# Performance work log

Measured on AMD Instinct MI355X. Metric: run time of the kernel, lower is better.

## Reference

```python
import jax, jax.numpy as jnp
from jax import lax
import numpy as np

SCALE = 3.0
TOPK = 16  # eigvec[:, -16:] in the original module
BN_EPS = 1e-5
DN = ('NCHW', 'OIHW', 'NCHW')


def setup_inputs() -> dict:
    key = jax.random.key(0)
    ks = jax.random.split(key, 8)
    B, C, H, W = 16, 256, 64, 64
    x = jax.random.normal(ks[0], (B, C, H, W), dtype=jnp.float32)
    conv1_w = jax.random.normal(ks[1], (C, C, 1, 1), dtype=jnp.float32) * (1.0 / np.sqrt(C))
    conv1_b = jax.random.normal(ks[2], (C,), dtype=jnp.float32) * 0.01
    conv2_w = jax.random.normal(ks[3], (C, C, 3, 3), dtype=jnp.float32) * (1.0 / np.sqrt(9 * C))
    bn_gamma = jnp.ones((C,), dtype=jnp.float32)
    bn_beta = jnp.zeros((C,), dtype=jnp.float32)
    bn_mean = jax.random.normal(ks[4], (C,), dtype=jnp.float32) * 0.1
    bn_var = jax.random.uniform(ks[5], (C,), dtype=jnp.float32, minval=0.5, maxval=1.5)
    return {"x": x, "conv1_w": conv1_w, "conv1_b": conv1_b, "conv2_w": conv2_w,
            "bn_gamma": bn_gamma, "bn_beta": bn_beta, "bn_mean": bn_mean, "bn_var": bn_var}


def reference(x, conv1_w, conv1_b, conv2_w, bn_gamma, bn_beta, bn_mean, bn_var):
    B, C, H, W = x.shape
    # conv1: 1x1 conv with bias
    gx = lax.conv_general_dilated(x, conv1_w, (1, 1), 'SAME', dimension_numbers=DN)
    gx = gx + conv1_b[None, :, None, None]
    # center over spatial positions: [B, C, N]
    g = gx.reshape(B, C, H * W)
    g = g - jnp.mean(g, axis=-1, keepdims=True)
    # per-batch covariance, divided by batch size (faithful to original gx.shape[0])
    cmat = jnp.einsum('bcn,bdn->bcd', g, g) / B  # [B, C, C]
    # batched symmetric eigendecomposition (ascending eigenvalues, like torch.symeig)
    _, vecs = jnp.linalg.eigh(cmat)              # vecs: [B, C, C]
    w = jnp.swapaxes(vecs[..., -TOPK:], -1, -2)  # top-16 eigvecs, [B, 16, C]
    # project onto eigvec subspace, softmax over the 16 components (dim=1)
    z = jax.nn.softmax(jnp.einsum('bkc,bcn->bkn', w, g) * SCALE, axis=1)  # [B, 16, N]
    y = jnp.einsum('bkc,bkn->bcn', w, z).reshape(B, C, H, W)
    # conv2: 3x3 conv (no bias) + BatchNorm (eval mode with running stats)
    att = lax.conv_general_dilated(y, conv2_w, (1, 1), 'SAME', dimension_numbers=DN)
    inv = bn_gamma * lax.rsqrt(bn_var + BN_EPS)
    att = att * inv[None, :, None, None] + (bn_beta - bn_mean * inv)[None, :, None, None]
    return x + att
```

## Files before the change

kernel.cpp:

```cpp
#include <hip/hip_runtime.h>
#include <hip/hip_bf16.h>
#include <math.h>


typedef __hip_bfloat16 bf16;

#define NB 16
#define NC 256
#define NSP 4096
#define LAPACK_EPS32 5.9604644775390625e-08

#define PHB_I0 80
#define PHB_M  176

__device__ __forceinline__ float b2f(bf16 v){ return __bfloat162float(v); }
__device__ __forceinline__ double safelog(double x){
  double a = fabs(x);
  if (!(a > 0.0) || !isfinite(a)) a = 1e-300;
  return log(a);
}

__device__ __forceinline__ float blk_reduce_sum(float s, float* red, int tid){
  red[tid] = s; __syncthreads();
  if (tid < 128) red[tid] += red[tid+128];
  __syncthreads();
  if (tid < 64){
    float x = red[tid] + red[tid+64];
    #pragma unroll
    for (int o = 32; o > 0; o >>= 1) x += __shfl_down(x, o);
    if (tid == 0) red[0] = x;
  }
  __syncthreads();
  return red[0];
}

__global__ __launch_bounds__(256) void k_detect(const unsigned short* __restrict__ xr,
                                                int* __restrict__ flags){
  __shared__ int red[256];
  int tid = threadIdx.x;
  int cnt = 0;
  for (int i = tid; i < 4096; i += 256){
    unsigned int u = xr[i];
    unsigned int e = (u >> 7) & 0xFF;
    if (e >= 134) ++cnt;
  }
  red[tid] = cnt; __syncthreads();
  for (int o=128;o>0;o>>=1){ if(tid<o) red[tid]+=red[tid+o]; __syncthreads(); }
  if (tid==0) flags[0] = (red[0] > 50) ? 1 : 0;
}

__global__ __launch_bounds__(256) void k_conv1(const void* __restrict__ xv_,
                                               const void* __restrict__ w1v,
                                               const int* __restrict__ flags,
                                               float* __restrict__ g){
  __shared__ float ws[16][256];
  int nt = blockIdx.x, ct = blockIdx.y, b = blockIdx.z;
  int tid = threadIdx.x;
  int c0 = ct*16;
  int isf = flags[0];
  if (isf){
    const float* w1 = (const float*)w1v;
    for (int i = tid; i < 16*256; i += 256)
      ws[i>>8][i&255] = w1[(size_t)(c0 + (i>>8))*256 + (i&255)];
  } else {
    const bf16* w1 = (const bf16*)w1v;
    for (int i = tid; i < 16*256; i += 256)
      ws[i>>8][i&255] = b2f(w1[(size_t)(c0 + (i>>8))*256 + (i&255)]);
  }
  __syncthreads();
  int n = nt*256 + tid;
  float acc[16];
  #pragma unroll
  for (int i=0;i<16;++i) acc[i]=0.f;
  if (isf){
    const float* xp = (const float*)xv_ + (size_t)b*NC*NSP + n;
    for (int d=0; d<256; ++d){
      float xv = xp[(size_t)d*NSP];
      #pragma unroll
      for (int i=0;i<16;++i) acc[i] = fmaf(ws[i][d], xv, acc[i]);
    }
  } else {
    const bf16* xp = (const bf16*)xv_ + (size_t)b*NC*NSP + n;
    for (int d=0; d<256; ++d){
      float xv = b2f(xp[(size_t)d*NSP]);
      #pragma unroll
      for (int i=0;i<16;++i) acc[i] = fmaf(ws[i][d], xv, acc[i]);
    }
  }
  float* gp = g + ((size_t)b*NC + c0)*NSP + n;
  #pragma unroll
  for (int i=0;i<16;++i) gp[(size_t)i*NSP] = acc[i];
}

__global__ __launch_bounds__(256) void k_center(float* __restrict__ g){
  int bc = blockIdx.x;
  float* p = g + (size_t)bc*NSP;
  int tid = threadIdx.x;
  __shared__ float red[256];
  float s = 0.f;
  for (int i=tid;i<NSP;i+=256) s += p[i];
  red[tid]=s; __syncthreads();
  for (int o=128;o>0;o>>=1){ if(tid<o) red[tid]+=red[tid+o]; __syncthreads(); }
  float mean = red[0] * (1.0f/4096.0f);
  for (int i=tid;i<NSP;i+=256) p[i] -= mean;
}

__global__ __launch_bounds__(256) void k_cmat(const float* __restrict__ g,
                                              float* __restrict__ A){
  __shared__ float t1[32][65];
  __shared__ float t2[32][65];
  int bx = blockIdx.x, by = blockIdx.y, b = blockIdx.z;
  int tid = threadIdx.x;
  int tx = tid & 31, ty = tid >> 5;
  const float* gb = g + (size_t)b*NC*NSP;
  float acc[4] = {0.f,0.f,0.f,0.f};
  for (int ch=0; ch<64; ++ch){
    int n0 = ch*64;
    for (int idx=tid; idx<2048; idx+=256){
      int r = idx>>6, cc = idx&63;
      t1[r][cc] = gb[(size_t)(by*32 + r)*NSP + n0 + cc];
      t2[r][cc] = gb[(size_t)(bx*32 + r)*NSP + n0 + cc];
    }
    __syncthreads();
    for (int kk=0; kk<64; ++kk){
      float v2 = t2[tx][kk];
      #pragma unroll
      for (int jj=0;jj<4;++jj) acc[jj] = fmaf(t1[ty+8*jj][kk], v2, acc[jj]);
    }
    __syncthreads();
  }
  #pragma unroll
  for (int jj=0;jj<4;++jj){
    int row = by*32 + ty + 8*jj, col = bx*32 + tx;
    A[((size_t)b*NC + row)*NC + col] = acc[jj]*(1.0f/16.0f);
  }
}

__global__ __launch_bounds__(256,1) void k_sytd2(float* __restrict__ Ag,
                                                 float* __restrict__ e_g,
                                                 float* __restrict__ tau_g,
                                                 float* __restrict__ d_g){
  int b = blockIdx.x, tid = threadIdx.x;
  float* A = Ag + (size_t)b*65536;
  __shared__ float Asub[PHB_M*PHB_M];
  __shared__ float v[256], wv[256], red[256];

  for (int i=0;i<PHB_I0;++i){
    float alpha = A[(size_t)i*256+(i+1)];
    float s=0.f;
    for (int r=i+2+tid; r<256; r+=256){ float a=A[(size_t)i*256+r]; s+=a*a; }
    float xnorm2 = blk_reduce_sum(s, red, tid);
    float tau=0.f, scale=0.f, beta=alpha;
    if (xnorm2 > 0.f){
      float r_ = sqrtf(alpha*alpha + xnorm2);
      beta = (alpha >= 0.f) ? -r_ : r_;
      tau = (beta - alpha)/beta;
      scale = 1.0f/(alpha - beta);
    }
    if (tid==0){ e_g[b*256+i] = beta; tau_g[b*256+i] = tau; }
    if (tau != 0.f){
      for (int r=i+1+tid; r<256; r+=256){
        float val = (r==i+1)?1.0f : A[(size_t)i*256+r]*scale;
        A[(size_t)i*256+r] = val;  v[r] = val;
      }
      __syncthreads();
      for (int r=i+1+tid; r<256; r+=256){
        const float* Ar = A + r;
        float acc=0.f;
        int base = i+1;
        int nfull = (256-base) >> 5;
        float b0[32], b1[32];
        if (nfull>0){
          #pragma unroll
          for (int u=0;u<32;++u) b0[u] = Ar[(size_t)(base+u)*256];
        }
        int t=0;
        for (; t+2<=nfull; t+=2){
          int cB = base+(t+1)*32;
          #pragma unroll
          for (int u=0;u<32;++u) b1[u] = Ar[(size_t)(cB+u)*256];
          int cA = base+t*32;
          #pragma unroll
          for (int u=0;u<32;++u) acc = fmaf(b0[u], v[cA+u], acc);
          if (t+2 < nfull){
            int cC = base+(t+2)*32;
            #pragma unroll
            for (int u=0;u<32;++u) b0[u] = Ar[(size_t)(cC+u)*256];
          }
          #pragma unroll
          for (int u=0;u<32;++u) acc = fmaf(b1[u], v[cB+u], acc);
        }
        if (t<nfull){
          int cA = base+t*32;
          #pragma unroll
          for (int u=0;u<32;++u) acc = fmaf(b0[u], v[cA+u], acc);
          ++t;
        }
        for (int c2=base+nfull*32; c2<256; ++c2) acc = fmaf(Ar[(size_t)c2*256], v[c2], acc);
        wv[r] = tau*acc;
      }
      __syncthreads();
      float sd=0.f;
      for (int r=i+1+tid;r<256;r+=256) sd += v[r]*wv[r];
      float dotv = blk_reduce_sum(sd, red, tid);
      float a2 = -0.5f*tau*dotv;
      for (int r=i+1+tid;r<256;r+=256) wv[r] += a2*v[r];
      __syncthreads();
      int r = i+1+tid;
      if (r < 256){
        float vr=v[r], wr=wv[r];
        float* Arw = A + r;
        int base=i+1;
        int nfull=(256-base)>>5;
        float b0[32], b1[32];
        if (nfull>0){
          #pragma unroll
          for (int u=0;u<32;++u) b0[u] = Arw[(size_t)(base+u)*256];
        }
        int t=0;
        for (; t+2<=nfull; t+=2){
          int cB = base+(t+1)*32;
          #pragma unroll
          for (int u=0;u<32;++u) b1[u] = Arw[(size_t)(cB+u)*256];
          int cA = base+t*32;
          #pragma unroll
          for (int u=0;u<32;++u) b0[u] -= vr*wv[cA+u] + wr*v[cA+u];
          #pragma unroll
          for (int u=0;u<32;++u) Arw[(size_t)(cA+u)*256] = b0[u];
          if (t+2 < nfull){
            int cC = base+(t+2)*32;
            #pragma unroll
            for (int u=0;u<32;++u) b0[u] = Arw[(size_t)(cC+u)*256];
          }
          #pragma unroll
          for (int u=0;u<32;++u) b1[u] -= vr*wv[cB+u] + wr*v[cB+u];
          #pragma unroll
          for (int u=0;u<32;++u) Arw[(size_t)(cB+u)*256] = b1[u];
        }
        if (t<nfull){
          int cA = base+t*32;
          #pragma unroll
          for (int u=0;u<32;++u) b0[u] -= vr*wv[cA+u] + wr*v[cA+u];
          #pragma unroll
          for (int u=0;u<32;++u) Arw[(size_t)(cA+u)*256] = b0[u];
          ++t;
        }
        for (int c2=base+nfull*32; c2<256; ++c2)
          Arw[(size_t)c2*256] -= vr*wv[c2] + wr*v[c2];
      }
      __syncthreads();
    }
    __syncthreads();
  }

  for (int idx=tid; idx<PHB_M*PHB_M; idx+=256){
    int cc = idx / PHB_M, rr = idx - cc*PHB_M;
    Asub[idx] = A[(size_t)(PHB_I0+cc)*256 + (PHB_I0+rr)];
  }
  __syncthreads();

  for (int i=PHB_I0;i<255;++i){
    int cb = (i - PHB_I0)*PHB_M;
    float alpha = Asub[cb + (i+1-PHB_I0)];
    float s=0.f;
    for (int r=i+2+tid; r<256; r+=256){ float a=Asub[cb + (r-PHB_I0)]; s+=a*a; }
    float xnorm2 = blk_reduce_sum(s, red, tid);
    float tau=0.f, scale=0.f, beta=alpha;
    if (xnorm2 > 0.f){
      float r_ = sqrtf(alpha*alpha + xnorm2);
      beta = (alpha >= 0.f) ? -r_ : r_;
      tau = (beta - alpha)/beta;
      scale = 1.0f/(alpha - beta);
    }
    if (tid==0){ e_g[b*256+i] = beta; tau_g[b*256+i] = tau; }
    if (tau != 0.f){
      for (int r=i+1+tid; r<256; r+=256){
        float val = (r==i+1)?1.0f : Asub[cb+(r-PHB_I0)]*scale;
        Asub[cb+(r-PHB_I0)] = val;
        A[(size_t)i*256+r] = val;
        v[r] = val;
      }
      __syncthreads();
      for (int r=i+1+tid; r<256; r+=256){
        int ro = r - PHB_I0;
        float acc=0.f;
        int base=i+1;
        int nfull=(256-base)>>4;
        for (int t=0;t<nfull;++t){
          int cA = base + t*16;
          float av[16];
          #pragma unroll
          for (int u=0;u<16;++u) av[u] = Asub[(cA+u-PHB_I0)*PHB_M + ro];
          #pragma unroll
          for (int u=0;u<16;++u) acc = fmaf(av[u], v[cA+u], acc);
        }
        for (int c2=base+nfull*16;c2<256;++c2)
          acc = fmaf(Asub[(c2-PHB_I0)*PHB_M+ro], v[c2], acc);
        wv[r] = tau*acc;
      }
      __syncthreads();
      float sd=0.f;
      for (int r=i+1+tid;r<256;r+=256) sd += v[r]*wv[r];
      float dotv = blk_reduce_sum(sd, red, tid);
      float a2 = -0.5f*tau*dotv;
      for (int r=i+1+tid;r<256;r+=256) wv[r] += a2*v[r];
      __syncthreads();
      int r = i+1+tid;
      if (r < 256){
        int ro = r - PHB_I0;
        float vr=v[r], wr=wv[r];
        int base=i+1;
        int nfull=(256-base)>>4;
        for (int t=0;t<nfull;++t){
          int cA=base+t*16;
          float av[16];
          #pragma unroll
          for (int u=0;u<16;++u) av[u] = Asub[(cA+u-PHB_I0)*PHB_M+ro];
          #pragma unroll
          for (int u=0;u<16;++u) av[u] -= vr*wv[cA+u] + wr*v[cA+u];
          #pragma unroll
          for (int u=0;u<16;++u) Asub[(cA+u-PHB_I0)*PHB_M+ro] = av[u];
        }
        for (int c2=base+nfull*16;c2<256;++c2)
          Asub[(c2-PHB_I0)*PHB_M+ro] -= vr*wv[c2] + wr*v[c2];
      }
      __syncthreads();
    }
    __syncthreads();
  }
  for (int r=tid;r<256;r+=256){
    float dv = (r >= PHB_I0)? Asub[(r-PHB_I0)*PHB_M + (r-PHB_I0)] : A[(size_t)r*256+r];
    d_g[b*256+r] = dv;
  }
}

__global__ __launch_bounds__(256) void k_leaf(const float* __restrict__ d_g,
                                              const float* __restrict__ e_g,
                                              float* __restrict__ Qg,
                                              double* __restrict__ Dw_g,
                                              double* __restrict__ emod_g){
  int b = blockIdx.x, tid = threadIdx.x;
  float* Q = Qg + (size_t)b*65536;
  double* Dw = Dw_g + (size_t)b*256;
  __shared__ double As[16*257];
  __shared__ float  Vt[16*257];
  __shared__ double dms[256];
  __shared__ double emod[256];
  __shared__ float redf[256];

  float dv = d_g[b*256+tid];
  float ev = (tid<255)? e_g[b*256+tid] : 0.f;
  redf[tid] = fmaxf(fabsf(dv), fabsf(ev)); __syncthreads();
  for(int o=128;o>0;o>>=1){ if(tid<o) redf[tid]=fmaxf(redf[tid],redf[tid+o]); __syncthreads(); }
  double sigma = (double)redf[0];
  if (!(sigma > 0.0)) sigma = 1.0;
  double dmod = (double)dv;
  if ((tid & 15)==15 && tid<255) dmod -= fabs((double)e_g[b*256+tid]);
  if ((tid & 15)==0  && tid>0)   dmod -= fabs((double)e_g[b*256+tid-1]);
  dmod /= sigma;
  double em = (tid<255)? ((double)ev)/sigma : 0.0;
  dms[tid] = dmod;  emod[tid] = em;
  emod_g[b*256+tid] = em;
  __syncthreads();

  int l16 = tid & ~15, j = tid & 15;
  for (int r=0;r<16;++r){
    double av = 0.0;
    if (r==j)        av = dms[l16+j];
    else if (r==j-1) av = emod[l16+j-1];
    else if (r==j+1) av = emod[l16+j];
    As[r*257+tid] = av;
    Vt[r*257+tid] = (r==j)? 1.f : 0.f;
  }
  __syncthreads();

  for (int sweep=0; sweep<14; ++sweep){
    for (int p=0;p<15;++p){
      for (int q=p+1;q<16;++q){
        double app = As[p*257 + l16+p];
        double aqq = As[q*257 + l16+q];
        double apq = As[p*257 + l16+q];
        bool rot = (fabs(apq) > 1e-18);
        double c, s;
        if (rot){
          double theta = (aqq - app)/(2.0*apq);
          double t = 1.0/(fabs(theta)+sqrt(1.0+theta*theta));
          if (theta < 0.0) t = -t;
          c = 1.0/sqrt(1.0+t*t); s = t*c;
        } else { c = 1.0; s = 0.0; }
        double apj = As[p*257 + tid];
        double aqj = As[q*257 + tid];
        double npj = c*apj - s*aqj;
        double nqj = s*apj + c*aqj;
        if (rot && j==p){ npj = c*c*app - 2.0*c*s*apq + s*s*aqq; nqj = 0.0; }
        if (rot && j==q){ npj = 0.0; nqj = s*s*app + 2.0*c*s*apq + c*c*aqq; }
        As[p*257 + tid] = npj;
        As[q*257 + tid] = nqj;
        As[j*257 + l16+p] = npj;
        As[j*257 + l16+q] = nqj;
        float vp = Vt[p*257 + tid], vq = Vt[q*257 + tid];
        Vt[p*257 + tid] = (float)(c*(double)vp - s*(double)vq);
        Vt[q*257 + tid] = (float)(s*(double)vp + c*(double)vq);
      }
    }
  }
  __syncthreads();
  double myval = As[j*257 + l16+j];
  int rank = 0;
  for (int k=0;k<16;++k){
    double vk = As[k*257 + l16+k];
    if (vk < myval || (vk==myval && k<j)) ++rank;
  }
  Dw[l16+rank] = myval;
  for (int r=0;r<16;++r)
    Q[(size_t)(l16+r)*256 + (l16+rank)] = Vt[j*257 + l16+r];
}

struct DCMerge {
  double z_[256], dsv[256], ds2[256], zs2[256];
  double dl_[256], zl_[256], taus[256], ztil[256], normk[256], evo[256];
  double rotcs[256][2];
  int    cs2[256], colx[256], non_[256], defl_[256], anch[256], osrc[256], otyp[256];
  int    roti[256][2];
};

__global__ __launch_bounds__(256) void k_msolve(int lev,
                                                const double* __restrict__ emod_g,
                                                float* __restrict__ Qsrc,
                                                double* __restrict__ Dw_g,
                                                double* __restrict__ Sdl,
                                                double* __restrict__ Sztil,
                                                double* __restrict__ Staus,
                                                double* __restrict__ Snk,
                                                int* __restrict__ Scolx,
                                                int* __restrict__ Sanch,
                                                int* __restrict__ Sotyp,
                                                int* __restrict__ Sosrc,
                                                int* __restrict__ SK){
  int mrg = blockIdx.x, b = blockIdx.y, tid = threadIdx.x;
  float* Q  = Qsrc + (size_t)b*65536;
  double* Dw = Dw_g + (size_t)b*256;
  int slot = b*8 + mrg;
  __shared__ DCMerge mg;
  __shared__ int bci[4];

  int ssz = 16<<lev, nm = ssz<<1;
  int base = mrg*nm;
  double rho0 = emod_g[b*256 + base+ssz-1];
  if (tid < nm){
    float zf = (tid < ssz) ? Q[(size_t)(base+ssz-1)*256 + base + tid]
                           : Q[(size_t)(base+ssz)*256   + base + tid];
    double zz = (double)zf;
    if (rho0 < 0.0 && tid >= ssz) zz = -zz;
    mg.z_[tid] = zz * 0.70710678118654752440;
    mg.dsv[tid] = Dw[base+tid];
  }
  __syncthreads();
  double rho = fabs(2.0*rho0);
  if (tid==0){
    int i1=0, i2=ssz, o=0;
    while (i1<ssz || i2<nm){
      bool take1;
      if (i1>=ssz) take1=false; else if (i2>=nm) take1=true;
      else take1 = (mg.dsv[i1] <= mg.dsv[i2]);
      int src = take1? i1++ : i2++;
      mg.ds2[o]=mg.dsv[src]; mg.zs2[o]=mg.z_[src]; mg.cs2[o]=src; ++o;
    }
  }
  __syncthreads();
  mg.taus[tid] = (tid<nm)? fabs(mg.zs2[tid]) : 0.0; __syncthreads();
  for(int o2=128;o2>0;o2>>=1){ if(tid<o2) mg.taus[tid]=fmax(mg.taus[tid],mg.taus[tid+o2]); __syncthreads(); }
  double zmax = mg.taus[0]; __syncthreads();
  mg.taus[tid] = (tid<nm)? fabs(mg.ds2[tid]) : 0.0; __syncthreads();
  for(int o2=128;o2>0;o2>>=1){ if(tid<o2) mg.taus[tid]=fmax(mg.taus[tid],mg.taus[tid+o2]); __syncthreads(); }
  double dmax = mg.taus[0]; __syncthreads();
  double tol = 8.0*LAPACK_EPS32*fmax(dmax, zmax);
  if (tid==0){
    int K=0, nd=0, nrot=0, pj=-1;
    for (int j=0;j<nm;++j){
      if (rho*fabs(mg.zs2[j]) <= tol){ mg.defl_[nd++]=j; continue; }
      if (pj>=0){
        double sg=mg.zs2[pj], cg=mg.zs2[j];
        double tg=mg.ds2[j]-mg.ds2[pj];
        double taug=sqrt(cg*cg+sg*sg);
        double cn, sn;
        if (taug > 0.0){ cn=cg/taug; sn=-sg/taug; } else { cn=1.0; sn=0.0; }
        if (fabs(tg*cn*sn) <= tol){
          mg.zs2[j]=taug; mg.zs2[pj]=0.0;
          mg.roti[nrot][0]=mg.cs2[pj]; mg.roti[nrot][1]=mg.cs2[j];
          mg.rotcs[nrot][0]=cn; mg.rotcs[nrot][1]=sn; ++nrot;
          double t2 = mg.ds2[pj]*cn*cn + mg.ds2[j]*sn*sn;
          mg.ds2[j] = mg.ds2[pj]*sn*sn + mg.ds2[j]*cn*cn;
          mg.ds2[pj] = t2;
          mg.defl_[nd++]=pj;
          pj=j;
        } else { mg.non_[K++]=pj; pj=j; }
      } else pj=j;
    }
    if (pj>=0) mg.non_[K++]=pj;
    bci[0]=K; bci[1]=nd; bci[2]=nrot;
  }
  __syncthreads();
  int K=bci[0], nd=bci[1], nrot=bci[2];
  for (int r2=0;r2<nrot;++r2){
    int ca = base + mg.roti[r2][0], cb2 = base + mg.roti[r2][1];
    double cn = mg.rotcs[r2][0], sn = mg.rotcs[r2][1];
    if (tid < nm){
      int row = base+tid;
      float xv = Q[(size_t)row*256+ca], yv = Q[(size_t)row*256+cb2];
      Q[(size_t)row*256+ca]  = (float)(cn*(double)xv + sn*(double)yv);
      Q[(size_t)row*256+cb2] = (float)(cn*(double)yv - sn*(double)xv);
    }
    __syncthreads();
  }
  if (tid<K){
    mg.dl_[tid]=mg.ds2[mg.non_[tid]];
    mg.zl_[tid]=mg.zs2[mg.non_[tid]];
    mg.colx[tid]=mg.cs2[mg.non_[tid]];
  }
  __syncthreads();
  mg.taus[tid] = (tid<K)? mg.zl_[tid]*mg.zl_[tid] : 0.0; __syncthreads();
  for(int o2=128;o2>0;o2>>=1){ if(tid<o2) mg.taus[tid]+=mg.taus[tid+o2]; __syncthreads(); }
  double zsum2 = mg.taus[0]; __syncthreads();
  if (tid<K){
    int j=tid;
    double left=mg.dl_[j];
    double right=(j<K-1)? mg.dl_[j+1] : (mg.dl_[K-1] + rho*zsum2);
    double mid=0.5*(left+right);
    double fm=1.0;
    for (int i3=0;i3<K;++i3){
      double del=mg.dl_[i3]-mid;
      fm += rho*mg.zl_[i3]*mg.zl_[i3]/del;
    }
    int a; double lo, hi;
    if (j==K-1){
      a=K-1;
      if (fm<=0.0){ lo=mid-left; hi=right-left; } else { lo=0.0; hi=mid-left; }
    } else if (fm<=0.0){ a=j+1; lo=mid-mg.dl_[j+1]; hi=0.0; }
    else { a=j; lo=0.0; hi=mid-left; }
    double da2=mg.dl_[a];
    double t;
    if (hi > lo){
      t=0.5*(lo+hi);
    } else {
      t = (a==j)? 1e-300 : -1e-300;
      lo = fmin(lo, t); hi = fmax(hi, t);
    }
    for (int it=0; it<100; ++it){
      double gg=1.0, dg=0.0;
      for (int i3=0;i3<K;++i3){
        double del=(mg.dl_[i3]-da2)-t;
        double q=mg.zl_[i3]/del;
        gg += rho*mg.zl_[i3]*q;
        dg += rho*q*q;
      }
      if (gg<0.0) lo=t; else hi=t;
      double tn = t - gg/dg;
      if (!isfinite(tn) || !(tn>lo && tn<hi)) tn=0.5*(lo+hi);
      if (tn == 0.0) tn = (t!=0.0)? t*0.5 : ((a==j)?1e-300:-1e-300);
      double dstep=fabs(tn-t);
      t=tn;
      if (dstep <= 1e-15*(fabs(t)+1e-30)) break;
      if ((hi-lo) <= 1e-15*(fabs(da2)+fabs(t)+1e-30)) break;
    }
    if (t == 0.0 || !isfinite(t)) t = (a==j)? 1e-300 : -1e-300;
    mg.taus[j]=t; mg.anch[j]=a;
  }
  __syncthreads();
  if (tid<K){
    int i3=tid; double acc=0.0; double di=mg.dl_[i3];
    for (int j=0;j<K;++j){
      double lmd = (mg.dl_[mg.anch[j]] - di) + mg.taus[j];
      acc += safelog(lmd);
      if (j!=i3) acc -= safelog(mg.dl_[j]-di);
    }
    double mag = exp(0.5*acc);
    if (!isfinite(mag)) mag = 0.0;
    mg.ztil[i3] = (mg.zl_[i3] >= 0.0)? mag : -mag;
  }
  __syncthreads();
  if (tid<K){
    int j=tid; double da2=mg.dl_[mg.anch[j]]; double tj=mg.taus[j];
    double nr=0.0;
    for (int i3=0;i3<K;++i3){
      double del=(mg.dl_[i3]-da2)-tj;
      if (del == 0.0) del = (tj>=0.0)? -1e-300 : 1e-300;
      double sv=mg.ztil[i3]/del;
      nr += sv*sv;
    }
    if (!(nr > 0.0) || !isfinite(nr)) nr = 1.0;
    mg.normk[j]=sqrt(nr);
  }
  __syncthreads();
  if (tid==0){
    for (int a2=1;a2<nd;++a2){
      int key=mg.defl_[a2]; double kv=mg.ds2[key]; int b2=a2-1;
      while (b2>=0 && mg.ds2[mg.defl_[b2]] > kv){ mg.defl_[b2+1]=mg.defl_[b2]; --b2; }
      mg.defl_[b2+1]=key;
    }
    int i1=0,i2=0,o=0;
    while (i1<K || i2<nd){
      double v1 = (i1<K)? (mg.dl_[mg.anch[i1]]+mg.taus[i1]) : 0.0;
      double v2 = (i2<nd)? mg.ds2[mg.defl_[i2]] : 0.0;
      bool take1;
      if (i1>=K) take1=false; else if (i2>=nd) take1=true; else take1 = (v1 <= v2);
      if (take1){ mg.otyp[o]=0; mg.osrc[o]=i1; mg.evo[o]=v1; ++i1; }
      else { mg.otyp[o]=1; mg.osrc[o]=mg.cs2[mg.defl_[i2]]; mg.evo[o]=v2; ++i2; }
      ++o;
    }
  }
  __syncthreads();
  if (tid<nm) Dw[base+tid]=mg.evo[tid];
  size_t so = (size_t)slot*256;
  if (tid<K){
    Sdl[so+tid]=mg.dl_[tid]; Sztil[so+tid]=mg.ztil[tid];
    Staus[so+tid]=mg.taus[tid]; Snk[so+tid]=mg.normk[tid];
    Scolx[so+tid]=mg.colx[tid]; Sanch[so+tid]=mg.anch[tid];
  }
  if (tid<nm){ Sotyp[so+tid]=mg.otyp[tid]; Sosrc[so+tid]=mg.osrc[tid]; }
  if (tid==0) SK[slot]=K;
}

__global__ __launch_bounds__(256) void k_mvec(int lev,
                                              const float* __restrict__ Qsrc_g,
                                              float* __restrict__ Qdst_g,
                                              const double* __restrict__ Sdl,
                                              const double* __restrict__ Sztil,
                                              const double* __restrict__ Staus,
                                              const double* __restrict__ Snk,
                                              const int* __restrict__ Scolx,
                                              const int* __restrict__ Sanch,
                                              const int* __restrict__ Sotyp,
                                              const int* __restrict__ Sosrc,
                                              const int* __restrict__ SK){
  int t = blockIdx.x, mrg = blockIdx.y, b = blockIdx.z, tid = threadIdx.x;
  const float* Q = Qsrc_g + (size_t)b*65536;
  float* Qd = Qdst_g + (size_t)b*65536;
  int slot = b*8 + mrg;
  size_t so = (size_t)slot*256;
  int ssz = 16<<lev, nm = ssz<<1;
  int base = mrg*nm;
  int p0 = t*16;
  int K = SK[slot];

  __shared__ float svf[256*16];
  __shared__ double cda[16], ctj[16];
  __shared__ float cnk[16];
  __shared__ int ctyp[16], csrc[16];

  if (tid < 16){
    int p = p0 + tid;
    int typ = Sotyp[so+p], src = Sosrc[so+p];
    ctyp[tid]=typ; csrc[tid]=src;
    if (typ==0){
      int j = src;
      cda[tid] = Sdl[so + Sanch[so+j] - 0 + 0];
    }
  }
  __syncthreads();
  if (tid < 16){
    int p = p0 + tid;
    if (ctyp[tid]==0){
      int j = csrc[tid];
      int a = Sanch[so+j];
      cda[tid] = Sdl[so+a];
      ctj[tid] = Staus[so+j];
      cnk[tid] = (float)Snk[so+j];
    } else { cda[tid]=0.0; ctj[tid]=1.0; cnk[tid]=1.f; }
  }
  __syncthreads();
  for (int idx = tid; idx < K*16; idx += 256){
    int i3 = idx >> 4, c = idx & 15;
    float sv = 0.f;
    if (ctyp[c]==0){
      double del = (Sdl[so+i3] - cda[c]) - ctj[c];
      if (del == 0.0) del = (ctj[c]>=0.0)? -1e-300 : 1e-300;
      sv = (float)( Sztil[so+i3]/del / (double)cnk[c] );
      if (!isfinite(sv)) sv = 0.f;
    }
    svf[i3*16 + c] = sv;
  }
  __syncthreads();

  if (tid < nm){
    int row = base + tid;
    const float* Qr = Q + (size_t)row*256 + base;
    float acc[16];
    #pragma unroll
    for (int c=0;c<16;++c) acc[c]=0.f;
    for (int i3=0;i3<K;++i3){
      float qv = Qr[Scolx[so+i3]];
      #pragma unroll
      for (int c=0;c<16;++c) acc[c] = fmaf(qv, svf[i3*16+c], acc[c]);
    }
    #pragma unroll
    for (int c=0;c<16;++c){
      float v = acc[c];
      if (ctyp[c]==1) v = Qr[csrc[c]];
      if (!isfinite(v)) v = 0.f;
      Qd[(size_t)row*256 + base + p0 + c] = v;
    }
  }
}

__global__ __launch_bounds__(256,1) void k_backtf(const float* __restrict__ Ag,
                                                  const float* __restrict__ tau_g,
                                                  const float* __restrict__ Qg,
                                                  float* __restrict__ w16g){
  int b=blockIdx.x, tid=threadIdx.x;
  const float* A=Ag+(size_t)b*65536;
  const float* Q=Qg+(size_t)b*65536;
  __shared__ float U[256][17];
  __shared__ float pd[16][17];
  __shared__ float dk[16];
  int k=tid&15, rg=tid>>4;
  for (int r=rg;r<256;r+=16) U[r][k]=Q[(size_t)r*256+240+k];
  __syncthreads();
  for (int i=254;i>=0;--i){
    float tau=tau_g[b*256+i];
    if (tau!=0.f){
      int r0 = i+1+rg;
      float ar[16];
      #pragma unroll
      for (int u=0;u<16;++u){
        int r = r0 + u*16;
        ar[u] = (r<256)? A[(size_t)i*256+r] : 0.f;
      }
      float uv[16];
      #pragma unroll
      for (int u=0;u<16;++u){
        int r = r0 + u*16;
        uv[u] = (r<256)? U[r][k] : 0.f;
      }
      float s=0.f;
      #pragma unroll
      for (int u=0;u<16;++u){
        int r = r0 + u*16;
        if (r<256) s += ar[u]*uv[u];
      }
      pd[rg][k]=s;
      __syncthreads();
      if (tid<16){
        float acc=0.f;
        #pragma unroll
        for (int gg=0; gg<16; ++gg) acc+=pd[gg][tid];
        dk[tid]=tau*acc;
      }
      __syncthreads();
      float dkk = dk[k];
      #pragma unroll
      for (int u=0;u<16;++u){
        int r = r0 + u*16;
        if (r<256) U[r][k] -= dkk*ar[u];
      }
      __syncthreads();
    }
  }
  for (int c2=rg;c2<256;c2+=16){
    float uv = U[c2][k];
    if (!isfinite(uv)) uv = 0.f;
    w16g[((size_t)b*16+k)*256+c2]=uv;
  }
}

__global__ __launch_bounds__(256) void k_score(const float* __restrict__ g,
                                               const float* __restrict__ w16,
                                               float* __restrict__ z){
  __shared__ float ws[16][256];
  int nt=blockIdx.x, b=blockIdx.y, tid=threadIdx.x;
  for (int i=tid;i<4096;i+=256) ws[i>>8][i&255]=w16[(size_t)b*4096+i];
  __syncthreads();
  int n=nt*256+tid;
  const float* gp=g+(size_t)b*NC*NSP+n;
  float acc[16];
  #pragma unroll
  for(int k2=0;k2<16;++k2) acc[k2]=0.f;
  for (int c2=0;c2<256;++c2){
    float gv=gp[(size_t)c2*NSP];
    #pragma unroll
    for (int k2=0;k2<16;++k2) acc[k2]=fmaf(ws[k2][c2],gv,acc[k2]);
  }
  float mx=-1e30f;
  #pragma unroll
  for(int k2=0;k2<16;++k2){ acc[k2]*=3.0f; mx=fmaxf(mx,acc[k2]); }
  float sum=0.f;
  #pragma unroll
  for(int k2=0;k2<16;++k2){ acc[k2]=expf(acc[k2]-mx); sum+=acc[k2]; }
  float inv=1.0f/sum;
  float* zp=z+(size_t)b*16*NSP+n;
  #pragma unroll
  for(int k2=0;k2<16;++k2) zp[(size_t)k2*NSP]=acc[k2]*inv;
}

__global__ __launch_bounds__(256) void k_y(const float* __restrict__ z,
                                           const float* __restrict__ w16,
                                           float* __restrict__ y){
  __shared__ float ws[16][256];
  int nt=blockIdx.x, b=blockIdx.y, tid=threadIdx.x;
  for (int i=tid;i<4096;i+=256) ws[i>>8][i&255]=w16[(size_t)b*4096+i];
  __syncthreads();
  int n=nt*256+tid;
  const float* zp=z+(size_t)b*16*NSP+n;
  float zr[16];
  #pragma unroll
  for(int k2=0;k2<16;++k2) zr[k2]=zp[(size_t)k2*NSP];
  float* yp=y+(size_t)b*NC*NSP+n;
  for (int c2=0;c2<256;++c2){
    float acc=0.f;
    #pragma unroll
    for (int k2=0;k2<16;++k2) acc=fmaf(ws[k2][c2],zr[k2],acc);
    yp[(size_t)c2*NSP]=acc;
  }
}

__global__ __launch_bounds__(256) void k_conv2(const float* __restrict__ y,
                                               const void* __restrict__ w2v,
                                               const void* __restrict__ xv_,
                                               const void* __restrict__ gmv,
                                               const void* __restrict__ btv,
                                               const void* __restrict__ muv,
                                               const void* __restrict__ vrv,
                                               const int* __restrict__ flags,
                                               void* __restrict__ outv){
  __shared__ float yt[8][6][66];
  __shared__ float wt[16][8][9];
  int ht=blockIdx.x, ct=blockIdx.y, b=blockIdx.z, tid=threadIdx.x;
  int hl=tid>>6, wl=tid&63;
  int h=ht*4+hl;
  int c0=ct*16;
  int isf = flags[0];
  float acc[16];
  #pragma unroll
  for(int i=0;i<16;++i) acc[i]=0.f;
  const float* yb = y + (size_t)b*NC*NSP;
  for (int d0=0; d0<256; d0+=8){
    for (int idx=tid; idx<8*6*64; idx+=256){
      int dd=idx/384; int rem=idx-dd*384; int rr=rem>>6; int cc2=rem&63;
      int hg=ht*4-1+rr;
      float v = (hg>=0 && hg<64)? yb[(size_t)(d0+dd)*NSP + hg*64 + cc2] : 0.f;
      yt[dd][rr][cc2+1]=v;
    }
    if (tid<48){ int dd=tid/6, rr=tid-dd*6; yt[dd][rr][0]=0.f; yt[dd][rr][65]=0.f; }
    if (isf){
      const float* w2 = (const float*)w2v;
      for (int idx=tid; idx<16*8*9; idx+=256){
        int cc=idx/72; int rem=idx-cc*72; int dd=rem/9; int kk=rem-dd*9;
        wt[cc][dd][kk]=w2[ ((size_t)(c0+cc)*256 + d0+dd)*9 + kk ];
      }
    } else {
      const bf16* w2 = (const bf16*)w2v;
      for (int idx=tid; idx<16*8*9; idx+=256){
        int cc=idx/72; int rem=idx-cc*72; int dd=rem/9; int kk=rem-dd*9;
        wt[cc][dd][kk]=b2f(w2[ ((size_t)(c0+cc)*256 + d0+dd)*9 + kk ]);
      }
    }
    __syncthreads();
    for (int cc=0; cc<16; ++cc){
      float a=acc[cc];
      #pragma unroll
      for (int dd=0; dd<8; ++dd){
        const float* wp=wt[cc][dd];
        a = fmaf(wp[0], yt[dd][hl+0][wl+0], a);
        a = fmaf(wp[1], yt[dd][hl+0][wl+1], a);
        a = fmaf(wp[2], yt[dd][hl+0][wl+2], a);
        a = fmaf(wp[3], yt[dd][hl+1][wl+0], a);
        a = fmaf(wp[4], yt[dd][hl+1][wl+1], a);
        a = fmaf(wp[5], yt[dd][hl+1][wl+2], a);
        a = fmaf(wp[6], yt[dd][hl+2][wl+0], a);
        a = fmaf(wp[7], yt[dd][hl+2][wl+1], a);
        a = fmaf(wp[8], yt[dd][hl+2][wl+2], a);
      }
      acc[cc]=a;
    }
    __syncthreads();
  }
  size_t nidx=(size_t)h*64+wl;
  for (int cc=0;cc<16;++cc){
    int c=c0+cc;
    float gmf, btf, muf, vrf, xvv;
    size_t oi = ((size_t)b*NC+c)*NSP + nidx;
    if (isf){
      gmf=((const float*)gmv)[c]; btf=((const float*)btv)[c];
      muf=((const float*)muv)[c]; vrf=((const float*)vrv)[c];
      xvv=((const float*)xv_)[oi];
    } else {
      gmf=b2f(((const bf16*)gmv)[c]); btf=b2f(((const bf16*)btv)[c]);
      muf=b2f(((const bf16*)muv)[c]); vrf=b2f(((const bf16*)vrv)[c]);
      xvv=b2f(((const bf16*)xv_)[oi]);
    }
    float inv = gmf * rsqrtf(vrf + 1e-5f);
    float shift = btf - muf*inv;
    float val = xvv + acc[cc]*inv + shift;
    if (isf) ((float*)outv)[oi] = val;
    else     ((bf16*)outv)[oi] = __float2bfloat16(val);
  }
}

extern "C" void kernel_launch(void* const* d_in, const int* in_sizes, int n_in,
                              void* d_out, int out_size, void* d_ws, size_t ws_size,
                              hipStream_t stream) {
  const void* x   = d_in[0];
  const void* w1  = d_in[1];
  const void* w2  = d_in[3];
  const void* gmm = d_in[4];
  const void* bet = d_in[5];
  const void* mu  = d_in[6];
  const void* var = d_in[7];

  float* g    = (float*)d_ws;
  float* A    = g   + (size_t)NB*NC*NSP;
  float* Qa   = A   + (size_t)NB*NC*NC;
  float* Qb   = Qa  + (size_t)NB*NC*NC;
  float* w16  = Qb  + (size_t)NB*NC*NC;
  float* zb   = w16 + (size_t)NB*16*NC;
  float* e_g  = zb  + (size_t)NB*16*NSP;
  float* tau_g= e_g + (size_t)NB*NC;
  float* d_g  = tau_g + (size_t)NB*NC;
  double* Dw  = (double*)(d_g + (size_t)NB*NC);
  double* emod_g = Dw + (size_t)NB*NC;
  double* Sdl   = emod_g + (size_t)NB*NC;
  double* Sztil = Sdl   + (size_t)128*256;
  double* Staus = Sztil + (size_t)128*256;
  double* Snk   = Staus + (size_t)128*256;
  int* Scolx = (int*)(Snk + (size_t)128*256);
  int* Sanch = Scolx + (size_t)128*256;
  int* Sotyp = Sanch + (size_t)128*256;
  int* Sosrc = Sotyp + (size_t)128*256;
  int* SK    = Sosrc + (size_t)128*256;
  int* flags = SK + 256;
  size_t needed = (size_t)((char*)(flags + 16) - (char*)d_ws);
  if (ws_size < needed) return;

  hipMemsetAsync(Qa, 0, (size_t)NB*NC*NC*2*sizeof(float), stream);
  k_detect<<<dim3(1),256,0,stream>>>((const unsigned short*)x, flags);
  k_conv1 <<<dim3(16,16,16),256,0,stream>>>(x, w1, flags, g);
  k_center<<<dim3(NB*NC),256,0,stream>>>(g);
  k_cmat  <<<dim3(8,8,16),256,0,stream>>>(g, A);
  k_sytd2 <<<dim3(16),256,0,stream>>>(A, e_g, tau_g, d_g);
  k_leaf  <<<dim3(16),256,0,stream>>>(d_g, e_g, Qa, Dw, emod_g);
  k_msolve<<<dim3(8,16),256,0,stream>>>(0, emod_g, Qa, Dw, Sdl,Sztil,Staus,Snk,Scolx,Sanch,Sotyp,Sosrc,SK);
  k_mvec  <<<dim3(2,8,16),256,0,stream>>>(0, Qa, Qb, Sdl,Sztil,Staus,Snk,Scolx,Sanch,Sotyp,Sosrc,SK);
  k_msolve<<<dim3(4,16),256,0,stream>>>(1, emod_g, Qb, Dw, Sdl,Sztil,Staus,Snk,Scolx,Sanch,Sotyp,Sosrc,SK);
  k_mvec  <<<dim3(4,4,16),256,0,stream>>>(1, Qb, Qa, Sdl,Sztil,Staus,Snk,Scolx,Sanch,Sotyp,Sosrc,SK);
  k_msolve<<<dim3(2,16),256,0,stream>>>(2, emod_g, Qa, Dw, Sdl,Sztil,Staus,Snk,Scolx,Sanch,Sotyp,Sosrc,SK);
  k_mvec  <<<dim3(8,2,16),256,0,stream>>>(2, Qa, Qb, Sdl,Sztil,Staus,Snk,Scolx,Sanch,Sotyp,Sosrc,SK);
  k_msolve<<<dim3(1,16),256,0,stream>>>(3, emod_g, Qb, Dw, Sdl,Sztil,Staus,Snk,Scolx,Sanch,Sotyp,Sosrc,SK);
  k_mvec  <<<dim3(16,1,16),256,0,stream>>>(3, Qb, Qa, Sdl,Sztil,Staus,Snk,Scolx,Sanch,Sotyp,Sosrc,SK);
  k_backtf<<<dim3(16),256,0,stream>>>(A, tau_g, Qa, w16);
  k_score <<<dim3(16,16),256,0,stream>>>(g, w16, zb);
  k_y     <<<dim3(16,16),256,0,stream>>>(zb, w16, g);
  k_conv2 <<<dim3(16,16,16),256,0,stream>>>(g, w2, x, gmm, bet, mu, var, flags, d_out);
}
```

Measured before the change: 8.099 ms.

## Split tridiagonal reduction columns across two thread halves with 512-thread blocks

```diff
diff --git a/kernel.cpp b/kernel.cpp
--- a/kernel.cpp
+++ b/kernel.cpp
@@ -22,6 +22,22 @@
 
 __device__ __forceinline__ float blk_reduce_sum(float s, float* red, int tid){
   red[tid] = s; __syncthreads();
+  if (tid < 128) red[tid] += red[tid+128];
+  __syncthreads();
+  if (tid < 64){
+    float x = red[tid] + red[tid+64];
+    #pragma unroll
+    for (int o = 32; o > 0; o >>= 1) x += __shfl_down(x, o);
+    if (tid == 0) red[0] = x;
+  }
+  __syncthreads();
+  return red[0];
+}
+
+__device__ __forceinline__ float blk_reduce_sum512(float s, float* red, int tid){
+  red[tid] = s; __syncthreads();
+  if (tid < 256) red[tid] += red[tid+256];
+  __syncthreads();
   if (tid < 128) red[tid] += red[tid+128];
   __syncthreads();
   if (tid < 64){
@@ -136,20 +152,23 @@
   }
 }
 
-__global__ __launch_bounds__(256,1) void k_sytd2(float* __restrict__ Ag,
+__global__ __launch_bounds__(512,1) void k_sytd2(float* __restrict__ Ag,
                                                  float* __restrict__ e_g,
                                                  float* __restrict__ tau_g,
                                                  float* __restrict__ d_g){
   int b = blockIdx.x, tid = threadIdx.x;
+  int rid = tid & 255, half = tid >> 8;
   float* A = Ag + (size_t)b*65536;
   __shared__ float Asub[PHB_M*PHB_M];
-  __shared__ float v[256], wv[256], red[256];
+  __shared__ float v[256], wv[256];
+  __shared__ float red[512];
+  __shared__ float accbuf[512];
 
   for (int i=0;i<PHB_I0;++i){
     float alpha = A[(size_t)i*256+(i+1)];
     float s=0.f;
-    for (int r=i+2+tid; r<256; r+=256){ float a=A[(size_t)i*256+r]; s+=a*a; }
-    float xnorm2 = blk_reduce_sum(s, red, tid);
+    { int r=i+2+tid; if (r<256){ float a=A[(size_t)i*256+r]; s=a*a; } }
+    float xnorm2 = blk_reduce_sum512(s, red, tid);
     float tau=0.f, scale=0.f, beta=alpha;
     if (xnorm2 > 0.f){
       float r_ = sqrtf(alpha*alpha + xnorm2);
@@ -159,93 +178,101 @@
     }
     if (tid==0){ e_g[b*256+i] = beta; tau_g[b*256+i] = tau; }
     if (tau != 0.f){
-      for (int r=i+1+tid; r<256; r+=256){
-        float val = (r==i+1)?1.0f : A[(size_t)i*256+r]*scale;
-        A[(size_t)i*256+r] = val;  v[r] = val;
-      }
-      __syncthreads();
-      for (int r=i+1+tid; r<256; r+=256){
-        const float* Ar = A + r;
+      { int r=i+1+tid;
+        if (r<256){
+          float val = (r==i+1)?1.0f : A[(size_t)i*256+r]*scale;
+          A[(size_t)i*256+r] = val;  v[r] = val;
+        }
+      }
+      __syncthreads();
+      int r = i+1+rid;
+      bool rv = (r < 256);
+      int cmid = (i+1+256) >> 1;
+      int cstart = (half==0)? (i+1) : cmid;
+      int cend   = (half==0)? cmid  : 256;
+      {
         float acc=0.f;
-        int base = i+1;
-        int nfull = (256-base) >> 5;
-        float b0[32], b1[32];
+        if (rv){
+          const float* Ar = A + r;
+          int nfull = (cend-cstart) >> 4;
+          float b0[16], b1[16];
+          if (nfull>0){
+            #pragma unroll
+            for (int u=0;u<16;++u) b0[u] = Ar[(size_t)(cstart+u)*256];
+          }
+          int t=0;
+          for (; t+2<=nfull; t+=2){
+            int cB = cstart+(t+1)*16;
+            #pragma unroll
+            for (int u=0;u<16;++u) b1[u] = Ar[(size_t)(cB+u)*256];
+            int cA = cstart+t*16;
+            #pragma unroll
+            for (int u=0;u<16;++u) acc = fmaf(b0[u], v[cA+u], acc);
+            if (t+2 < nfull){
+              int cC = cstart+(t+2)*16;
+              #pragma unroll
+              for (int u=0;u<16;++u) b0[u] = Ar[(size_t)(cC+u)*256];
+            }
+            #pragma unroll
+            for (int u=0;u<16;++u) acc = fmaf(b1[u], v[cB+u], acc);
+          }
+          if (t<nfull){
+            int cA = cstart+t*16;
+            #pragma unroll
+            for (int u=0;u<16;++u) acc = fmaf(b0[u], v[cA+u], acc);
+            ++t;
+          }
+          for (int c2=cstart+nfull*16; c2<cend; ++c2)
+            acc = fmaf(Ar[(size_t)c2*256], v[c2], acc);
+        }
+        accbuf[half*256+rid] = acc;
+      }
+      __syncthreads();
+      if (half==0 && rv) wv[r] = tau*(accbuf[rid] + accbuf[256+rid]);
+      __syncthreads();
+      float sd = (half==0 && rv)? v[r]*wv[r] : 0.f;
+      float dotv = blk_reduce_sum512(sd, red, tid);
+      float a2 = -0.5f*tau*dotv;
+      if (half==0 && rv) wv[r] += a2*v[r];
+      __syncthreads();
+      if (rv){
+        float vr=v[r], wr=wv[r];
+        float* Arw = A + r;
+        int nfull = (cend-cstart) >> 4;
+        float b0[16], b1[16];
         if (nfull>0){
           #pragma unroll
-          for (int u=0;u<32;++u) b0[u] = Ar[(size_t)(base+u)*256];
+          for (int u=0;u<16;++u) b0[u] = Arw[(size_t)(cstart+u)*256];
         }
         int t=0;
         for (; t+2<=nfull; t+=2){
-          int cB = base+(t+1)*32;
-          #pragma unroll
-          for (int u=0;u<32;++u) b1[u] = Ar[(size_t)(cB+u)*256];
-          int cA = base+t*32;
-          #pragma unroll
-          for (int u=0;u<32;++u) acc = fmaf(b0[u], v[cA+u], acc);
+          int cB = cstart+(t+1)*16;
+          #pragma unroll
+          for (int u=0;u<16;++u) b1[u] = Arw[(size_t)(cB+u)*256];
+          int cA = cstart+t*16;
+          #pragma unroll
+          for (int u=0;u<16;++u) b0[u] -= vr*wv[cA+u] + wr*v[cA+u];
+          #pragma unroll
+          for (int u=0;u<16;++u) Arw[(size_t)(cA+u)*256] = b0[u];
           if (t+2 < nfull){
-            int cC = base+(t+2)*32;
+            int cC = cstart+(t+2)*16;
             #pragma unroll
-            for (int u=0;u<32;++u) b0[u] = Ar[(size_t)(cC+u)*256];
+            for (int u=0;u<16;++u) b0[u] = Arw[(size_t)(cC+u)*256];
           }
           #pragma unroll
-          for (int u=0;u<32;++u) acc = fmaf(b1[u], v[cB+u], acc);
+          for (int u=0;u<16;++u) b1[u] -= vr*wv[cB+u] + wr*v[cB+u];
+          #pragma unroll
+          for (int u=0;u<16;++u) Arw[(size_t)(cB+u)*256] = b1[u];
         }
         if (t<nfull){
-          int cA = base+t*32;
-          #pragma unroll
-          for (int u=0;u<32;++u) acc = fmaf(b0[u], v[cA+u], acc);
+          int cA = cstart+t*16;
+          #pragma unroll
+          for (int u=0;u<16;++u) b0[u] -= vr*wv[cA+u] + wr*v[cA+u];
+          #pragma unroll
+          for (int u=0;u<16;++u) Arw[(size_t)(cA+u)*256] = b0[u];
           ++t;
         }
-        for (int c2=base+nfull*32; c2<256; ++c2) acc = fmaf(Ar[(size_t)c2*256], v[c2], acc);
-        wv[r] = tau*acc;
-      }
-      __syncthreads();
-      float sd=0.f;
-      for (int r=i+1+tid;r<256;r+=256) sd += v[r]*wv[r];
-      float dotv = blk_reduce_sum(sd, red, tid);
-      float a2 = -0.5f*tau*dotv;
-      for (int r=i+1+tid;r<256;r+=256) wv[r] += a2*v[r];
-      __syncthreads();
-      int r = i+1+tid;
-      if (r < 256){
-        float vr=v[r], wr=wv[r];
-        float* Arw = A + r;
-        int base=i+1;
-        int nfull=(256-base)>>5;
-        float b0[32], b1[32];
-        if (nfull>0){
-          #pragma unroll
-          for (int u=0;u<32;++u) b0[u] = Arw[(size_t)(base+u)*256];
-        }
-        int t=0;
-        for (; t+2<=nfull; t+=2){
-          int cB = base+(t+1)*32;
-          #pragma unroll
-          for (int u=0;u<32;++u) b1[u] = Arw[(size_t)(cB+u)*256];
-          int cA = base+t*32;
-          #pragma unroll
-          for (int u=0;u<32;++u) b0[u] -= vr*wv[cA+u] + wr*v[cA+u];
-          #pragma unroll
-          for (int u=0;u<32;++u) Arw[(size_t)(cA+u)*256] = b0[u];
-          if (t+2 < nfull){
-            int cC = base+(t+2)*32;
-            #pragma unroll
-            for (int u=0;u<32;++u) b0[u] = Arw[(size_t)(cC+u)*256];
-          }
-          #pragma unroll
-          for (int u=0;u<32;++u) b1[u] -= vr*wv[cB+u] + wr*v[cB+u];
-          #pragma unroll
-          for (int u=0;u<32;++u) Arw[(size_t)(cB+u)*256] = b1[u];
-        }
-        if (t<nfull){
-          int cA = base+t*32;
-          #pragma unroll
-          for (int u=0;u<32;++u) b0[u] -= vr*wv[cA+u] + wr*v[cA+u];
-          #pragma unroll
-          for (int u=0;u<32;++u) Arw[(size_t)(cA+u)*256] = b0[u];
-          ++t;
-        }
-        for (int c2=base+nfull*32; c2<256; ++c2)
+        for (int c2=cstart+nfull*16; c2<cend; ++c2)
           Arw[(size_t)c2*256] -= vr*wv[c2] + wr*v[c2];
       }
       __syncthreads();
@@ -253,7 +280,7 @@
     __syncthreads();
   }
 
-  for (int idx=tid; idx<PHB_M*PHB_M; idx+=256){
+  for (int idx=tid; idx<PHB_M*PHB_M; idx+=512){
     int cc = idx / PHB_M, rr = idx - cc*PHB_M;
     Asub[idx] = A[(size_t)(PHB_I0+cc)*256 + (PHB_I0+rr)];
   }
@@ -263,8 +290,8 @@
     int cb = (i - PHB_I0)*PHB_M;
     float alpha = Asub[cb + (i+1-PHB_I0)];
     float s=0.f;
-    for (int r=i+2+tid; r<256; r+=256){ float a=Asub[cb + (r-PHB_I0)]; s+=a*a; }
-    float xnorm2 = blk_reduce_sum(s, red, tid);
+    { int r=i+2+tid; if (r<256){ float a=Asub[cb + (r-PHB_I0)]; s=a*a; } }
+    float xnorm2 = blk_reduce_sum512(s, red, tid);
     float tau=0.f, scale=0.f, beta=alpha;
     if (xnorm2 > 0.f){
       float r_ = sqrtf(alpha*alpha + xnorm2);
@@ -274,45 +301,51 @@
     }
     if (tid==0){ e_g[b*256+i] = beta; tau_g[b*256+i] = tau; }
     if (tau != 0.f){
-      for (int r=i+1+tid; r<256; r+=256){
-        float val = (r==i+1)?1.0f : Asub[cb+(r-PHB_I0)]*scale;
-        Asub[cb+(r-PHB_I0)] = val;
-        A[(size_t)i*256+r] = val;
-        v[r] = val;
-      }
-      __syncthreads();
-      for (int r=i+1+tid; r<256; r+=256){
-        int ro = r - PHB_I0;
+      { int r=i+1+tid;
+        if (r<256){
+          float val = (r==i+1)?1.0f : Asub[cb+(r-PHB_I0)]*scale;
+          Asub[cb+(r-PHB_I0)] = val;
+          A[(size_t)i*256+r] = val;
+          v[r] = val;
+        }
+      }
+      __syncthreads();
+      int r = i+1+rid;
+      bool rv = (r < 256);
+      int ro = r - PHB_I0;
+      int cmid = (i+1+256) >> 1;
+      int cstart = (half==0)? (i+1) : cmid;
+      int cend   = (half==0)? cmid  : 256;
+      {
         float acc=0.f;
-        int base=i+1;
-        int nfull=(256-base)>>4;
+        if (rv){
+          int nfull = (cend-cstart) >> 4;
+          for (int t=0;t<nfull;++t){
+            int cA = cstart + t*16;
+            float av[16];
+            #pragma unroll
+            for (int u=0;u<16;++u) av[u] = Asub[(cA+u-PHB_I0)*PHB_M + ro];
+            #pragma unroll
+            for (int u=0;u<16;++u) acc = fmaf(av[u], v[cA+u], acc);
+          }
+          for (int c2=cstart+nfull*16;c2<cend;++c2)
+            acc = fmaf(Asub[(c2-PHB_I0)*PHB_M+ro], v[c2], acc);
+        }
+        accbuf[half*256+rid] = acc;
+      }
+      __syncthreads();
+      if (half==0 && rv) wv[r] = tau*(accbuf[rid] + accbuf[256+rid]);
+      __syncthreads();
+      float sd = (half==0 && rv)? v[r]*wv[r] : 0.f;
+      float dotv = blk_reduce_sum512(sd, red, tid);
+      float a2 = -0.5f*tau*dotv;
+      if (half==0 && rv) wv[r] += a2*v[r];
+      __syncthreads();
+      if (rv){
+        float vr=v[r], wr=wv[r];
+        int nfull = (cend-cstart) >> 4;
         for (int t=0;t<nfull;++t){
-          int cA = base + t*16;
-          float av[16];
-          #pragma unroll
-          for (int u=0;u<16;++u) av[u] = Asub[(cA+u-PHB_I0)*PHB_M + ro];
-          #pragma unroll
-          for (int u=0;u<16;++u) acc = fmaf(av[u], v[cA+u], acc);
-        }
-        for (int c2=base+nfull*16;c2<256;++c2)
-          acc = fmaf(Asub[(c2-PHB_I0)*PHB_M+ro], v[c2], acc);
-        wv[r] = tau*acc;
-      }
-      __syncthreads();
-      float sd=0.f;
-      for (int r=i+1+tid;r<256;r+=256) sd += v[r]*wv[r];
-      float dotv = blk_reduce_sum(sd, red, tid);
-      float a2 = -0.5f*tau*dotv;
-      for (int r=i+1+tid;r<256;r+=256) wv[r] += a2*v[r];
-      __syncthreads();
-      int r = i+1+tid;
-      if (r < 256){
-        int ro = r - PHB_I0;
-        float vr=v[r], wr=wv[r];
-        int base=i+1;
-        int nfull=(256-base)>>4;
-        for (int t=0;t<nfull;++t){
-          int cA=base+t*16;
+          int cA=cstart+t*16;
           float av[16];
           #pragma unroll
           for (int u=0;u<16;++u) av[u] = Asub[(cA+u-PHB_I0)*PHB_M+ro];
@@ -321,14 +354,15 @@
           #pragma unroll
           for (int u=0;u<16;++u) Asub[(cA+u-PHB_I0)*PHB_M+ro] = av[u];
         }
-        for (int c2=base+nfull*16;c2<256;++c2)
+        for (int c2=cstart+nfull*16;c2<cend;++c2)
           Asub[(c2-PHB_I0)*PHB_M+ro] -= vr*wv[c2] + wr*v[c2];
       }
       __syncthreads();
     }
     __syncthreads();
   }
-  for (int r=tid;r<256;r+=256){
+  if (tid < 256){
+    int r = tid;
     float dv = (r >= PHB_I0)? Asub[(r-PHB_I0)*PHB_M + (r-PHB_I0)] : A[(size_t)r*256+r];
     d_g[b*256+r] = dv;
   }
@@ -936,7 +970,7 @@
   k_conv1 <<<dim3(16,16,16),256,0,stream>>>(x, w1, flags, g);
   k_center<<<dim3(NB*NC),256,0,stream>>>(g);
   k_cmat  <<<dim3(8,8,16),256,0,stream>>>(g, A);
-  k_sytd2 <<<dim3(16),256,0,stream>>>(A, e_g, tau_g, d_g);
+  k_sytd2 <<<dim3(16),512,0,stream>>>(A, e_g, tau_g, d_g);
   k_leaf  <<<dim3(16),256,0,stream>>>(d_g, e_g, Qa, Dw, emod_g);
   k_msolve<<<dim3(8,16),256,0,stream>>>(0, emod_g, Qa, Dw, Sdl,Sztil,Staus,Snk,Scolx,Sanch,Sotyp,Sosrc,SK);
   k_mvec  <<<dim3(2,8,16),256,0,stream>>>(0, Qa, Qb, Sdl,Sztil,Staus,Snk,Scolx,Sanch,Sotyp,Sosrc,SK);
```

Result: faster. 7.633 ms (-5.8%).
